# Optimization experiments

Measured on AMD Instinct MI355X. Metric: run time of the kernel, lower is better.

Reference implementation:

```python
import jax, jax.numpy as jnp
import numpy as np

B, T, D, H, FF, E = 4, 1024, 1024, 16, 4096, 8
HD = D // H
EPS = 1e-5


def layernorm(x, g, b):
    mu = jnp.mean(x, axis=-1, keepdims=True)
    var = jnp.mean(jnp.square(x - mu), axis=-1, keepdims=True)
    return (x - mu) * jax.lax.rsqrt(var + EPS) * g + b


def setup_inputs() -> dict:
    key = jax.random.key(0)
    ks = jax.random.split(key, 24)
    s = 0.02
    inp = {
        "src": jax.random.normal(ks[0], (B, T, D), jnp.float32),
        "frac": jax.random.uniform(ks[1], (B, T), jnp.float32),
        "Wq": jax.random.normal(ks[2], (D, D), jnp.float32) * s,
        "bq": jnp.zeros((D,), jnp.float32),
        "Wk": jax.random.normal(ks[3], (D, D), jnp.float32) * s,
        "bk": jnp.zeros((D,), jnp.float32),
        "Wv": jax.random.normal(ks[4], (D, D), jnp.float32) * s,
        "bv": jnp.zeros((D,), jnp.float32),
        "Wo": jax.random.normal(ks[5], (D, D), jnp.float32) * s,
        "bo": jnp.zeros((D,), jnp.float32),
        "alpha_pos": jax.random.normal(ks[6], (H,), jnp.float32) * s,
        "alpha_neg": jax.random.normal(ks[7], (H,), jnp.float32) * s,
        "gate_W": jax.random.normal(ks[8], (D, E), jnp.float32) * s,
        "gate_b": jnp.zeros((E,), jnp.float32),
        "W1": jax.random.normal(ks[9], (E, D, FF), jnp.float32) * s,
        "b1": jnp.zeros((E, FF), jnp.float32),
        "W2": jax.random.normal(ks[10], (E, FF, D), jnp.float32) * s,
        "b2": jnp.zeros((E, D), jnp.float32),
        "ln1_g": jnp.ones((D,), jnp.float32),
        "ln1_b": jnp.zeros((D,), jnp.float32),
        "ln2_g": jnp.ones((D,), jnp.float32),
        "ln2_b": jnp.zeros((D,), jnp.float32),
    }
    return inp


def reference(src, frac, Wq, bq, Wk, bk, Wv, bv, Wo, bo, alpha_pos, alpha_neg,
              gate_W, gate_b, W1, b1, W2, b2, ln1_g, ln1_b, ln2_g, ln2_b):
    # ---- attention with per-head stoichiometric bias ----
    q = (src @ Wq + bq).reshape(B, T, H, HD).transpose(0, 2, 1, 3)  # [B,H,T,hd]
    k = (src @ Wk + bk).reshape(B, T, H, HD).transpose(0, 2, 1, 3)
    v = (src @ Wv + bv).reshape(B, T, H, HD).transpose(0, 2, 1, 3)
    scale = HD ** -0.5
    scores = jnp.einsum('bhqd,bhkd->bhqk', q, k) * scale  # [B,H,T,T]
    Dm = frac[:, None, :] - frac[:, :, None]  # frac_j - frac_i, [B,T,T]
    bias = (alpha_pos[None, :, None, None] * jax.nn.relu(Dm)[:, None]
            - alpha_neg[None, :, None, None] * jax.nn.relu(-Dm)[:, None])
    probs = jax.nn.softmax(scores + bias, axis=-1)
    attn = jnp.einsum('bhqk,bhkd->bhqd', probs, v)
    attn = attn.transpose(0, 2, 1, 3).reshape(B, T, D) @ Wo + bo

    x = layernorm(src + attn, ln1_g, ln1_b)

    # ---- top-2 MoE FFN ----
    logits = x @ gate_W + gate_b  # [B,T,E]
    gscores = jax.nn.softmax(logits, axis=-1)
    top2_scores, top2_idx = jax.lax.top_k(gscores, 2)  # [B,T,2]
    # dense per-expert combine weight: score if expert in top-2 else 0
    weights = jnp.sum(jax.nn.one_hot(top2_idx, E, dtype=x.dtype)
                      * top2_scores[..., None], axis=-2)  # [B,T,E]
    ff = jnp.zeros_like(x)
    for e in range(E):  # small fixed expert count
        h = jax.nn.relu(x @ W1[e] + b1[e])
        ff = ff + weights[..., e:e + 1] * (h @ W2[e] + b2[e])

    return layernorm(x + ff, ln2_g, ln2_b)
```

## Files before the change

### kernel.cpp

```cpp
#include <hip/hip_runtime.h>
#include <stdint.h>

typedef unsigned short u16;
typedef unsigned int   u32;

using bf16x8 = __attribute__((ext_vector_type(8))) short;
using f32x4  = __attribute__((ext_vector_type(4))) float;

#define N_T   1024
#define N_D   1024
#define N_E   8
#define N_BT  4096
#define LNEPS 1e-5f

__device__ __forceinline__ u32 rne2(float a, float b) {
  u32 ua = __float_as_uint(a); ua = (ua + 0x7fffu + ((ua >> 16) & 1u)) >> 16;
  u32 ub = __float_as_uint(b); ub = (ub + 0x7fffu + ((ub >> 16) & 1u)) >> 16;
  return ua | (ub << 16);
}
__device__ __forceinline__ u16 rne1(float a) {
  u32 ua = __float_as_uint(a);
  return (u16)((ua + 0x7fffu + ((ua >> 16) & 1u)) >> 16);
}
__device__ __forceinline__ float bfhi_f(float a) {
  u32 ua = __float_as_uint(a);
  ua = (ua + 0x7fffu + ((ua >> 16) & 1u)) & 0xffff0000u;
  return __uint_as_float(ua);
}
__device__ __forceinline__ int fch(int row) { return (row & 3) ^ ((row >> 2) & 3); }
__device__ __forceinline__ int swz(int row, int chunk) {
  return row * 32 + (((chunk ^ fch(row)) & 3) << 3);
}
__device__ __forceinline__ float wred(float v) {
  #pragma unroll
  for (int o2 = 32; o2 > 0; o2 >>= 1) v += __shfl_xor(v, o2, 64);
  return v;
}
__device__ __forceinline__ f32x4 mfma16(bf16x8 a, bf16x8 b, f32x4 c) {
  return __builtin_amdgcn_mfma_f32_16x16x32_bf16(a, b, c, 0, 0, 0);
}
typedef __attribute__((address_space(1))) const u32 gas_u32;
typedef __attribute__((address_space(3))) u32 las_u32;
__device__ __forceinline__ void gl16(const void* g, void* l) {
  __builtin_amdgcn_global_load_lds((gas_u32*)g, (las_u32*)l, 16, 0, 0);
}

template<int SPLIT>
__global__ __launch_bounds__(256)
void transpose_bf16(const float* __restrict__ in, u16* __restrict__ outh,
                    u16* __restrict__ outl, int R, int C, float scale)
{
  __shared__ u16 th[64][68];
  __shared__ u16 tl[SPLIT ? 64 : 1][SPLIT ? 68 : 1];
  const long long zb = (long long)blockIdx.z * R * C;
  const float* srcp = in + zb;
  const int r0 = blockIdx.y * 64, c0 = blockIdx.x * 64;
  const int t = threadIdx.x;
  {
    const int rr = t >> 4, cc = (t & 15) << 2;
    #pragma unroll
    for (int i = 0; i < 4; i++) {
      const int r = rr + i * 16;
      float4 v = *(const float4*)(srcp + (long long)(r0 + r) * C + c0 + cc);
      v.x *= scale; v.y *= scale; v.z *= scale; v.w *= scale;
      if constexpr (SPLIT) {
        float hx = bfhi_f(v.x), hy = bfhi_f(v.y), hz = bfhi_f(v.z), hw = bfhi_f(v.w);
        *(uint2*)&th[r][cc] = make_uint2(rne2(hx, hy), rne2(hz, hw));
        *(uint2*)&tl[r][cc] = make_uint2(rne2(v.x - hx, v.y - hy), rne2(v.z - hz, v.w - hw));
      } else {
        *(uint2*)&th[r][cc] = make_uint2(rne2(v.x, v.y), rne2(v.z, v.w));
      }
    }
  }
  __syncthreads();
  {
    const int c = t >> 2, rs = (t & 3) << 4;
    const long long ob = zb + (long long)(c0 + c) * R + r0 + rs;
    u32 w[8];
    #pragma unroll
    for (int i = 0; i < 8; i++)
      w[i] = (u32)th[rs + 2*i][c] | ((u32)th[rs + 2*i + 1][c] << 16);
    *(uint4*)(outh + ob)     = make_uint4(w[0], w[1], w[2], w[3]);
    *(uint4*)(outh + ob + 8) = make_uint4(w[4], w[5], w[6], w[7]);
    if constexpr (SPLIT) {
      #pragma unroll
      for (int i = 0; i < 8; i++)
        w[i] = (u32)tl[rs + 2*i][c] | ((u32)tl[rs + 2*i + 1][c] << 16);
      *(uint4*)(outl + ob)     = make_uint4(w[0], w[1], w[2], w[3]);
      *(uint4*)(outl + ob + 8) = make_uint4(w[4], w[5], w[6], w[7]);
    }
  }
}

__global__ __launch_bounds__(256)
void bias_cat(const float* __restrict__ bq, const float* __restrict__ bk,
              const float* __restrict__ bv, float* __restrict__ bcat)
{
  const int i = blockIdx.x * 256 + threadIdx.x;
  if (i < 1024)       bcat[i] = bq[i] * 0.125f;
  else if (i < 2048)  bcat[i] = bk[i - 1024];
  else if (i < 3072)  bcat[i] = bv[i - 2048];
}

__global__ __launch_bounds__(256)
void vtrans_bf16(const u16* __restrict__ Vh, const u16* __restrict__ Vl, int ldv,
                 u16* __restrict__ Vth, u16* __restrict__ Vtl)
{
  __shared__ u16 th[64][72];
  __shared__ u16 tl[64][72];
  const int bh = blockIdx.y, b = bh >> 4, h = bh & 15;
  const int kt = blockIdx.x, tid = threadIdx.x;
  {
    const int sr = tid >> 2, scb = (tid & 3) << 4;
    const long long off = (long long)(b * N_T + kt * 64 + sr) * ldv + h * 64 + scb;
    const uint4* vh = (const uint4*)(Vh + off);
    const uint4* vl = (const uint4*)(Vl + off);
    *(uint4*)&th[sr][scb]     = vh[0];
    *(uint4*)&th[sr][scb + 8] = vh[1];
    *(uint4*)&tl[sr][scb]     = vl[0];
    *(uint4*)&tl[sr][scb + 8] = vl[1];
  }
  __syncthreads();
  {
    const int od = tid >> 2, os0 = (tid & 3) << 4;
    u16 wh[16], wl[16];
    #pragma unroll
    for (int i = 0; i < 16; i++) { wh[i] = th[os0 + i][od]; wl[i] = tl[os0 + i][od]; }
    u16* oph = Vth + (long long)(bh * 64 + od) * N_T + kt * 64 + os0;
    u16* opl = Vtl + (long long)(bh * 64 + od) * N_T + kt * 64 + os0;
    *(uint4*)oph = make_uint4((u32)wh[0] | ((u32)wh[1] << 16), (u32)wh[2] | ((u32)wh[3] << 16),
                              (u32)wh[4] | ((u32)wh[5] << 16), (u32)wh[6] | ((u32)wh[7] << 16));
    *(uint4*)(oph + 8) = make_uint4((u32)wh[8] | ((u32)wh[9] << 16), (u32)wh[10] | ((u32)wh[11] << 16),
                                    (u32)wh[12] | ((u32)wh[13] << 16), (u32)wh[14] | ((u32)wh[15] << 16));
    *(uint4*)opl = make_uint4((u32)wl[0] | ((u32)wl[1] << 16), (u32)wl[2] | ((u32)wl[3] << 16),
                              (u32)wl[4] | ((u32)wl[5] << 16), (u32)wl[6] | ((u32)wl[7] << 16));
    *(uint4*)(opl + 8) = make_uint4((u32)wl[8] | ((u32)wl[9] << 16), (u32)wl[10] | ((u32)wl[11] << 16),
                                    (u32)wl[12] | ((u32)wl[13] << 16), (u32)wl[14] | ((u32)wl[15] << 16));
  }
}

template<int ASPLIT, int GATHER, int DORELU, int DOSCALE, int OBF, int GROUPED, int CG>
__global__ __launch_bounds__(256, 2)
void gemm128(const void* __restrict__ Ap, int lda,
             const u16* __restrict__ Bhp, const u16* __restrict__ Blp,
             long long bstride,
             void* __restrict__ Cp, int ldc,
             const float* __restrict__ biasp, int bias_stride,
             const float* __restrict__ slot_wp,
             const int* __restrict__ tokidx,
             const int2* __restrict__ tilesp, const int* __restrict__ ntilesp,
             int Ksz, void* __restrict__ Cp2, float cscale)
{
  const int gx = gridDim.x, nwg = gx * gridDim.y;
  const int orig = blockIdx.y * gx + blockIdx.x;
  const int flat = (orig & 7) * (nwg >> 3) + (orig >> 3);
  const int cgsz = gx * CG;
  const int colg = flat / cgsz, rem = flat % cgsz;
  const int bxx = rem / CG;
  const int byy = colg * CG + rem % CG;

  int e = 0, row0;
  if constexpr (GROUPED) {
    if (bxx >= *ntilesp) return;
    const int2 dsc = tilesp[bxx];
    e = dsc.x; row0 = dsc.y;
  } else {
    row0 = bxx * 128;
  }
  const int col0 = byy * 128;

  __shared__ __align__(16) u16 AhS[ASPLIT ? 1 : 2][128 * 32];
  __shared__ __align__(16) u16 BhS[ASPLIT ? 1 : 2][128 * 32];
  __shared__ __align__(16) u16 AlS[ASPLIT ? 128 * 32 : 8];
  __shared__ __align__(16) u16 BlS[ASPLIT ? 128 * 32 : 8];

  const int tid = threadIdx.x, wid = tid >> 6, lane = tid & 63;
  const int wm = (wid >> 1) << 6, wn = (wid & 1) << 6;
  const int l15 = lane & 15, l4 = lane >> 4;

  const int srow0 = wid * 32 + (lane >> 2);
  const int srow1 = srow0 + 16;
  const int sg0 = ((lane & 3) ^ fch(srow0)) << 3;
  const int sg1 = ((lane & 3) ^ fch(srow1)) << 3;
  const int lo0 = wid * 1024, lo1 = wid * 1024 + 512;

  const u16* Bg0 = Bhp + (long long)e * bstride + (long long)(col0 + srow0) * Ksz + sg0;
  const u16* Bg1 = Bhp + (long long)e * bstride + (long long)(col0 + srow1) * Ksz + sg1;
  const u16* Blg0 = nullptr; const u16* Blg1 = nullptr;
  if constexpr (ASPLIT) {
    Blg0 = Blp + (long long)e * bstride + (long long)(col0 + srow0) * Ksz + sg0;
    Blg1 = Blp + (long long)e * bstride + (long long)(col0 + srow1) * Ksz + sg1;
  }

  const u16* Ag0 = nullptr; const u16* Ag1 = nullptr;
  if constexpr (!ASPLIT) {
    long long ar0, ar1;
    if constexpr (GATHER) { ar0 = tokidx[row0 + srow0]; ar1 = tokidx[row0 + srow1]; }
    else                  { ar0 = row0 + srow0;          ar1 = row0 + srow1; }
    Ag0 = (const u16*)Ap + ar0 * (long long)lda + sg0;
    Ag1 = (const u16*)Ap + ar1 * (long long)lda + sg1;
  }

  f32x4 acc[4][4] = {};
  const int nk = Ksz >> 5;

  if constexpr (!ASPLIT) {
    gl16(Ag0, &AhS[0][lo0]); gl16(Ag1, &AhS[0][lo1]);
    gl16(Bg0, &BhS[0][lo0]); gl16(Bg1, &BhS[0][lo1]);
    asm volatile("s_waitcnt vmcnt(0)" ::: "memory");
    __syncthreads();
    int cur = 0;
    for (int kt = 0; kt < nk; kt++) {
      if (kt + 1 < nk) {
        const int ko = (kt + 1) << 5;
        gl16(Ag0 + ko, &AhS[cur ^ 1][lo0]);
        gl16(Ag1 + ko, &AhS[cur ^ 1][lo1]);
        gl16(Bg0 + ko, &BhS[cur ^ 1][lo0]);
        gl16(Bg1 + ko, &BhS[cur ^ 1][lo1]);
      }
      bf16x8 ah[4], bh[4];
      #pragma unroll
      for (int i = 0; i < 4; i++) {
        ah[i] = *(const bf16x8*)&AhS[cur][swz(wm + i * 16 + l15, l4)];
        bh[i] = *(const bf16x8*)&BhS[cur][swz(wn + i * 16 + l15, l4)];
      }
      #pragma unroll
      for (int i = 0; i < 4; i++)
        #pragma unroll
        for (int j = 0; j < 4; j++)
          acc[i][j] = mfma16(ah[i], bh[j], acc[i][j]);
      asm volatile("s_waitcnt vmcnt(0)" ::: "memory");
      __syncthreads();
      cur ^= 1;
    }
  } else {
    const int prr = tid >> 1, pc2 = (tid & 1) << 1;
    const float* Arow = (const float*)Ap + (long long)(row0 + prr) * lda;
    uint4 sah0, sah1, sal0, sal1;
    auto gloadA = [&](int k0) {
      const float4* ap = (const float4*)(Arow + k0 + pc2 * 8);
      float4 f0 = ap[0], f1 = ap[1], f2 = ap[2], f3 = ap[3];
      float h0 = bfhi_f(f0.x), h1 = bfhi_f(f0.y), h2 = bfhi_f(f0.z), h3 = bfhi_f(f0.w);
      float h4 = bfhi_f(f1.x), h5 = bfhi_f(f1.y), h6 = bfhi_f(f1.z), h7 = bfhi_f(f1.w);
      sah0 = make_uint4(rne2(h0, h1), rne2(h2, h3), rne2(h4, h5), rne2(h6, h7));
      sal0 = make_uint4(rne2(f0.x - h0, f0.y - h1), rne2(f0.z - h2, f0.w - h3),
                        rne2(f1.x - h4, f1.y - h5), rne2(f1.z - h6, f1.w - h7));
      h0 = bfhi_f(f2.x); h1 = bfhi_f(f2.y); h2 = bfhi_f(f2.z); h3 = bfhi_f(f2.w);
      h4 = bfhi_f(f3.x); h5 = bfhi_f(f3.y); h6 = bfhi_f(f3.z); h7 = bfhi_f(f3.w);
      sah1 = make_uint4(rne2(h0, h1), rne2(h2, h3), rne2(h4, h5), rne2(h6, h7));
      sal1 = make_uint4(rne2(f2.x - h0, f2.y - h1), rne2(f2.z - h2, f2.w - h3),
                        rne2(f3.x - h4, f3.y - h5), rne2(f3.z - h6, f3.w - h7));
    };
    gloadA(0);
    for (int kt = 0; kt < nk; kt++) {
      __syncthreads();
      const int ko = kt << 5;
      *(uint4*)&AhS[0][swz(prr, pc2)]     = sah0;
      *(uint4*)&AhS[0][swz(prr, pc2 + 1)] = sah1;
      *(uint4*)&AlS[swz(prr, pc2)]        = sal0;
      *(uint4*)&AlS[swz(prr, pc2 + 1)]    = sal1;
      gl16(Bg0 + ko, &BhS[0][lo0]);
      gl16(Bg1 + ko, &BhS[0][lo1]);
      gl16(Blg0 + ko, &BlS[lo0]);
      gl16(Blg1 + ko, &BlS[lo1]);
      asm volatile("s_waitcnt vmcnt(0)" ::: "memory");
      __syncthreads();
      if (kt + 1 < nk) gloadA((kt + 1) << 5);

      bf16x8 ah[4], bh[4], al[4], bl[4];
      #pragma unroll
      for (int i = 0; i < 4; i++) {
        const int ar = wm + i * 16 + l15;
        const int br = wn + i * 16 + l15;
        ah[i] = *(const bf16x8*)&AhS[0][swz(ar, l4)];
        bh[i] = *(const bf16x8*)&BhS[0][swz(br, l4)];
        al[i] = *(const bf16x8*)&AlS[swz(ar, l4)];
        bl[i] = *(const bf16x8*)&BlS[swz(br, l4)];
      }
      #pragma unroll
      for (int i = 0; i < 4; i++) {
        #pragma unroll
        for (int j = 0; j < 4; j++) {
          acc[i][j] = mfma16(ah[i], bh[j], acc[i][j]);
          acc[i][j] = mfma16(ah[i], bl[j], acc[i][j]);
          acc[i][j] = mfma16(al[i], bh[j], acc[i][j]);
        }
      }
    }
  }

  #pragma unroll
  for (int i = 0; i < 4; i++) {
    #pragma unroll
    for (int j = 0; j < 4; j++) {
      const int orow0 = row0 + wm + i * 16 + (l4 << 2);
      const int ocol  = col0 + wn + j * 16 + l15;
      const float bv = biasp[(long long)e * bias_stride + col0 + wn + j * 16 + l15];
      #pragma unroll
      for (int q = 0; q < 4; q++) {
        float v = acc[i][j][q] + bv;
        if constexpr (DORELU) v = fmaxf(v, 0.f);
        const long long orow = orow0 + q;
        if constexpr (DOSCALE) v *= slot_wp[orow];
        if constexpr (OBF == 2) {
          const float vs = v * cscale;
          const float hi = bfhi_f(vs);
          ((u16*)Cp )[orow * ldc + ocol] = (u16)(__float_as_uint(hi) >> 16);
          ((u16*)Cp2)[orow * ldc + ocol] = rne1(vs - hi);
        } else if constexpr (OBF == 1) {
          ((u16*)Cp)[orow * ldc + ocol] = rne1(v);
        } else {
          ((float*)Cp)[orow * ldc + ocol] = v;
        }
      }
    }
  }
}

__global__ __launch_bounds__(256, 2)
void attn_mfma(const u16* __restrict__ Qh, const u16* __restrict__ Ql,
               const u16* __restrict__ Kh, const u16* __restrict__ Kl, int ldq,
               const u16* __restrict__ Vth, const u16* __restrict__ Vtl,
               const float* __restrict__ frac,
               const float* __restrict__ apos, const float* __restrict__ aneg,
               float* __restrict__ ctx)
{
  __shared__ __align__(16) u16 KhS[64 * 64];
  __shared__ __align__(16) u16 KlS[64 * 64];
  __shared__ __align__(16) u16 VhS[64 * 64];
  __shared__ __align__(16) u16 VlS[64 * 64];
  __shared__ __align__(16) u16 PS[4][32][72];
  __shared__ __align__(16) float fjS[64];

  const int bh = blockIdx.x, b = bh >> 4, h = bh & 15;
  const int tid = threadIdx.x, wid = tid >> 6, lane = tid & 63;
  const int l15 = lane & 15, l4 = lane >> 4;
  const int q0 = blockIdx.y * 128 + wid * 32;

  bf16x8 qh[2][2], ql[2][2];
  #pragma unroll
  for (int ni = 0; ni < 2; ni++) {
    const long long qoff = (long long)(b * N_T + q0 + ni * 16 + l15) * ldq + h * 64 + l4 * 8;
    #pragma unroll
    for (int ks = 0; ks < 2; ks++) {
      qh[ni][ks] = *(const bf16x8*)(Qh + qoff + ks * 32);
      ql[ni][ks] = *(const bf16x8*)(Ql + qoff + ks * 32);
    }
  }
  float fq[2];
  #pragma unroll
  for (int ni = 0; ni < 2; ni++) fq[ni] = frac[b * N_T + q0 + ni * 16 + l15];
  const float ap = apos[h], an = aneg[h];

  f32x4 acc[4][2] = {};
  float mrun[2] = {-3.0e38f, -3.0e38f}, lrun[2] = {0.f, 0.f};

  const int sr = tid >> 2, scb = (tid & 3) << 4;
  const int ch0 = ((scb >> 3) ^ (sr & 7)) << 3;
  const int ch1 = (((scb >> 3) + 1) ^ (sr & 7)) << 3;

  for (int kt = 0; kt < 16; kt++) {
    __syncthreads();
    {
      const long long koff = (long long)(b * N_T + kt * 64 + sr) * ldq + h * 64 + scb;
      const uint4* khp = (const uint4*)(Kh + koff);
      const uint4* klp = (const uint4*)(Kl + koff);
      const long long voff = (long long)(bh * 64 + sr) * N_T + kt * 64 + scb;
      const uint4* vhp = (const uint4*)(Vth + voff);
      const uint4* vlp = (const uint4*)(Vtl + voff);
      *(uint4*)&KhS[sr * 64 + ch0] = khp[0];
      *(uint4*)&KhS[sr * 64 + ch1] = khp[1];
      *(uint4*)&KlS[sr * 64 + ch0] = klp[0];
      *(uint4*)&KlS[sr * 64 + ch1] = klp[1];
      *(uint4*)&VhS[sr * 64 + ch0] = vhp[0];
      *(uint4*)&VhS[sr * 64 + ch1] = vhp[1];
      *(uint4*)&VlS[sr * 64 + ch0] = vlp[0];
      *(uint4*)&VlS[sr * 64 + ch1] = vlp[1];
    }
    if (tid < 64) fjS[tid] = frac[b * N_T + kt * 64 + tid];
    __syncthreads();

    f32x4 s[4][2] = {};
    #pragma unroll
    for (int ks = 0; ks < 2; ks++) {
      bf16x8 kh[4], kl[4];
      #pragma unroll
      for (int mj = 0; mj < 4; mj++) {
        const int row = mj * 16 + l15;
        const int ch = (((ks << 2) + l4) ^ (row & 7)) << 3;
        kh[mj] = *(const bf16x8*)&KhS[row * 64 + ch];
        kl[mj] = *(const bf16x8*)&KlS[row * 64 + ch];
      }
      #pragma unroll
      for (int mj = 0; mj < 4; mj++) {
        #pragma unroll
        for (int ni = 0; ni < 2; ni++) {
          s[mj][ni] = mfma16(kh[mj], qh[ni][ks], s[mj][ni]);
          s[mj][ni] = mfma16(kh[mj], ql[ni][ks], s[mj][ni]);
          s[mj][ni] = mfma16(kl[mj], qh[ni][ks], s[mj][ni]);
        }
      }
    }

    #pragma unroll
    for (int mj = 0; mj < 4; mj++) {
      const int kvb = mj * 16 + l4 * 4;
      const float f0 = fjS[kvb], f1 = fjS[kvb + 1], f2 = fjS[kvb + 2], f3 = fjS[kvb + 3];
      #pragma unroll
      for (int ni = 0; ni < 2; ni++) {
        float d0 = f0 - fq[ni], d1 = f1 - fq[ni], d2 = f2 - fq[ni], d3 = f3 - fq[ni];
        s[mj][ni][0] += (d0 > 0.f ? ap : an) * d0;
        s[mj][ni][1] += (d1 > 0.f ? ap : an) * d1;
        s[mj][ni][2] += (d2 > 0.f ? ap : an) * d2;
        s[mj][ni][3] += (d3 > 0.f ? ap : an) * d3;
      }
    }

    #pragma unroll
    for (int ni = 0; ni < 2; ni++) {
      float tm = s[0][ni][0];
      #pragma unroll
      for (int mj = 0; mj < 4; mj++) {
        tm = fmaxf(tm, fmaxf(fmaxf(s[mj][ni][0], s[mj][ni][1]),
                             fmaxf(s[mj][ni][2], s[mj][ni][3])));
      }
      tm = fmaxf(tm, __shfl_xor(tm, 16, 64));
      tm = fmaxf(tm, __shfl_xor(tm, 32, 64));
      const float nm = fmaxf(mrun[ni], tm);
      const float cor = __expf(mrun[ni] - nm);
      mrun[ni] = nm;
      lrun[ni] *= cor;
      #pragma unroll
      for (int md = 0; md < 4; md++) {
        acc[md][ni][0] *= cor; acc[md][ni][1] *= cor;
        acc[md][ni][2] *= cor; acc[md][ni][3] *= cor;
      }
      float rsum = 0.f;
      #pragma unroll
      for (int mj = 0; mj < 4; mj++) {
        #pragma unroll
        for (int r = 0; r < 4; r++) {
          const float p = __expf(s[mj][ni][r] - nm);
          s[mj][ni][r] = p;
          rsum += p;
        }
      }
      rsum += __shfl_xor(rsum, 16, 64);
      rsum += __shfl_xor(rsum, 32, 64);
      lrun[ni] += rsum;
    }

    #pragma unroll
    for (int ni = 0; ni < 2; ni++) {
      #pragma unroll
      for (int mj = 0; mj < 4; mj++) {
        float h0 = bfhi_f(s[mj][ni][0]), h1 = bfhi_f(s[mj][ni][1]);
        float h2 = bfhi_f(s[mj][ni][2]), h3 = bfhi_f(s[mj][ni][3]);
        u32* dst = (u32*)&PS[wid][ni * 16 + l15][mj * 16 + l4 * 4];
        dst[0] = rne2(h0, h1); dst[1] = rne2(h2, h3);
      }
    }
    bf16x8 pbh[2][2];
    #pragma unroll
    for (int ni = 0; ni < 2; ni++)
      #pragma unroll
      for (int ks = 0; ks < 2; ks++)
        pbh[ni][ks] = *(const bf16x8*)&PS[wid][ni * 16 + l15][ks * 32 + l4 * 8];

    #pragma unroll
    for (int ni = 0; ni < 2; ni++) {
      #pragma unroll
      for (int mj = 0; mj < 4; mj++) {
        float p0 = s[mj][ni][0], p1 = s[mj][ni][1], p2 = s[mj][ni][2], p3 = s[mj][ni][3];
        float h0 = bfhi_f(p0), h1 = bfhi_f(p1), h2 = bfhi_f(p2), h3 = bfhi_f(p3);
        u32* dst = (u32*)&PS[wid][ni * 16 + l15][mj * 16 + l4 * 4];
        dst[0] = rne2(p0 - h0, p1 - h1); dst[1] = rne2(p2 - h2, p3 - h3);
      }
    }
    bf16x8 pbl[2][2];
    #pragma unroll
    for (int ni = 0; ni < 2; ni++)
      #pragma unroll
      for (int ks = 0; ks < 2; ks++)
        pbl[ni][ks] = *(const bf16x8*)&PS[wid][ni * 16 + l15][ks * 32 + l4 * 8];

    #pragma unroll
    for (int md = 0; md < 4; md++) {
      #pragma unroll
      for (int ks = 0; ks < 2; ks++) {
        const int row = md * 16 + l15;
        const int ch = (((ks << 2) + l4) ^ (row & 7)) << 3;
        const bf16x8 vh = *(const bf16x8*)&VhS[row * 64 + ch];
        const bf16x8 vl = *(const bf16x8*)&VlS[row * 64 + ch];
        #pragma unroll
        for (int nq = 0; nq < 2; nq++) {
          acc[md][nq] = mfma16(vh, pbh[nq][ks], acc[md][nq]);
          acc[md][nq] = mfma16(vh, pbl[nq][ks], acc[md][nq]);
          acc[md][nq] = mfma16(vl, pbh[nq][ks], acc[md][nq]);
        }
      }
    }
  }

  const float inv[2] = {1.f / lrun[0], 1.f / lrun[1]};
  #pragma unroll
  for (int nq = 0; nq < 2; nq++) {
    #pragma unroll
    for (int md = 0; md < 4; md++) {
      float4 o;
      o.x = acc[md][nq][0] * inv[nq];
      o.y = acc[md][nq][1] * inv[nq];
      o.z = acc[md][nq][2] * inv[nq];
      o.w = acc[md][nq][3] * inv[nq];
      *(float4*)(ctx + (long long)(b * N_T + q0 + nq * 16 + l15) * N_D +
                 h * 64 + md * 16 + l4 * 4) = o;
    }
  }
}

__global__ __launch_bounds__(256, 4)
void ln1_gate(const float* __restrict__ src, const float* __restrict__ attnout,
              const float* __restrict__ g, const float* __restrict__ bb,
              const float* __restrict__ gateW, const float* __restrict__ gateb,
              float* __restrict__ xout, u16* __restrict__ xbf,
              int2* __restrict__ tok_top, float2* __restrict__ tok_w)
{
  const int wid = threadIdx.x >> 6, lane = threadIdx.x & 63;
  const int t = blockIdx.x * 4 + wid;
  const float4* s4 = (const float4*)(src + (long long)t * N_D);
  const float4* a4 = (const float4*)(attnout + (long long)t * N_D);
  float4 v[4];
  float sum = 0.f;
  #pragma unroll
  for (int c = 0; c < 4; c++) {
    const int idx = c * 64 + lane;
    float4 a = s4[idx], b2 = a4[idx];
    v[c] = make_float4(a.x + b2.x, a.y + b2.y, a.z + b2.z, a.w + b2.w);
    sum += v[c].x + v[c].y + v[c].z + v[c].w;
  }
  sum = wred(sum);
  const float mu = sum * (1.f / 1024.f);
  float s2 = 0.f;
  #pragma unroll
  for (int c = 0; c < 4; c++) {
    float dx = v[c].x - mu, dy = v[c].y - mu, dz = v[c].z - mu, dw = v[c].w - mu;
    s2 += dx * dx + dy * dy + dz * dz + dw * dw;
  }
  s2 = wred(s2);
  const float rs = rsqrtf(s2 * (1.f / 1024.f) + LNEPS);
  float acc[8];
  #pragma unroll
  for (int e2 = 0; e2 < 8; e2++) acc[e2] = 0.f;
  #pragma unroll
  for (int c = 0; c < 4; c++) {
    const int idx = c * 64 + lane;
    float4 gv = ((const float4*)g)[idx], bv = ((const float4*)bb)[idx];
    float xa[4];
    xa[0] = (v[c].x - mu) * rs * gv.x + bv.x;
    xa[1] = (v[c].y - mu) * rs * gv.y + bv.y;
    xa[2] = (v[c].z - mu) * rs * gv.z + bv.z;
    xa[3] = (v[c].w - mu) * rs * gv.w + bv.w;
    ((float4*)(xout + (long long)t * N_D))[idx] = make_float4(xa[0], xa[1], xa[2], xa[3]);
    *(uint2*)&xbf[(long long)t * N_D + idx * 4] =
        make_uint2(rne2(xa[0], xa[1]), rne2(xa[2], xa[3]));
    #pragma unroll
    for (int ii = 0; ii < 4; ii++) {
      const float xs = xa[ii];
      const float4* gw = (const float4*)(gateW + ((long long)(idx * 4 + ii)) * N_E);
      float4 w0 = gw[0], w1 = gw[1];
      acc[0] += xs * w0.x; acc[1] += xs * w0.y; acc[2] += xs * w0.z; acc[3] += xs * w0.w;
      acc[4] += xs * w1.x; acc[5] += xs * w1.y; acc[6] += xs * w1.z; acc[7] += xs * w1.w;
    }
  }
  #pragma unroll
  for (int e2 = 0; e2 < 8; e2++) acc[e2] = wred(acc[e2]);
  if (lane == 0) {
    float lg[8];
    #pragma unroll
    for (int e2 = 0; e2 < 8; e2++) lg[e2] = acc[e2] + gateb[e2];
    float mx = lg[0];
    #pragma unroll
    for (int e2 = 1; e2 < 8; e2++) mx = fmaxf(mx, lg[e2]);
    float Z = 0.f;
    #pragma unroll
    for (int e2 = 0; e2 < 8; e2++) Z += __expf(lg[e2] - mx);
    int e0 = 0; float v0 = lg[0];
    #pragma unroll
    for (int e2 = 1; e2 < 8; e2++) if (lg[e2] > v0) { v0 = lg[e2]; e0 = e2; }
    int e1 = -1; float v1 = -3.4e38f;
    #pragma unroll
    for (int e2 = 0; e2 < 8; e2++) if (e2 != e0 && lg[e2] > v1) { v1 = lg[e2]; e1 = e2; }
    tok_top[t] = make_int2(e0, e1);
    tok_w[t] = make_float2(__expf(v0 - mx) / Z, __expf(v1 - mx) / Z);
  }
}

__global__ __launch_bounds__(256)
void route_build(const int2* __restrict__ tok_top, int* __restrict__ offsets,
                 int* __restrict__ cursors, int* __restrict__ ntiles,
                 int2* __restrict__ tiles, int* __restrict__ token_idx,
                 float* __restrict__ slot_w)
{
  __shared__ int cnt[N_E];
  __shared__ int soff[N_E + 1];
  __shared__ int scnt[N_E];
  const int tid = threadIdx.x;
  if (tid < N_E) cnt[tid] = 0;
  __syncthreads();
  int lc0 = 0, lc1 = 0, lc2 = 0, lc3 = 0, lc4 = 0, lc5 = 0, lc6 = 0, lc7 = 0;
  for (int t = tid; t < N_BT; t += 256) {
    const int2 ee = tok_top[t];
    lc0 += (ee.x == 0) + (ee.y == 0); lc1 += (ee.x == 1) + (ee.y == 1);
    lc2 += (ee.x == 2) + (ee.y == 2); lc3 += (ee.x == 3) + (ee.y == 3);
    lc4 += (ee.x == 4) + (ee.y == 4); lc5 += (ee.x == 5) + (ee.y == 5);
    lc6 += (ee.x == 6) + (ee.y == 6); lc7 += (ee.x == 7) + (ee.y == 7);
  }
  if (lc0) atomicAdd(&cnt[0], lc0); if (lc1) atomicAdd(&cnt[1], lc1);
  if (lc2) atomicAdd(&cnt[2], lc2); if (lc3) atomicAdd(&cnt[3], lc3);
  if (lc4) atomicAdd(&cnt[4], lc4); if (lc5) atomicAdd(&cnt[5], lc5);
  if (lc6) atomicAdd(&cnt[6], lc6); if (lc7) atomicAdd(&cnt[7], lc7);
  __syncthreads();
  if (tid == 0) {
    int off = 0, nt = 0;
    for (int ex = 0; ex < N_E; ex++) {
      soff[ex] = off; offsets[ex] = off; cursors[ex] = 0;
      const int c = cnt[ex];
      scnt[ex] = c;
      const int pt = (c + 127) >> 7;
      for (int i = 0; i < pt; i++) { tiles[nt] = make_int2(ex, off + i * 128); nt++; }
      off += pt << 7;
    }
    soff[N_E] = off; offsets[N_E] = off;
    *ntiles = nt;
  }
  __syncthreads();
  for (int ex = 0; ex < N_E; ex++)
    for (int s = soff[ex] + scnt[ex] + tid; s < soff[ex + 1]; s += 256) {
      token_idx[s] = 0; slot_w[s] = 0.f;
    }
}

__global__ __launch_bounds__(256)
void route_scatter(const int2* __restrict__ tok_top, const float2* __restrict__ tok_w,
                   const int* __restrict__ offsets, int* __restrict__ cursors,
                   int* __restrict__ token_idx, float* __restrict__ slot_w,
                   int* __restrict__ slotA, int* __restrict__ slotB)
{
  const int t = blockIdx.x * 256 + threadIdx.x;
  if (t >= N_BT) return;
  const int2 ee = tok_top[t];
  const float2 ww = tok_w[t];
  int p = atomicAdd(&cursors[ee.x], 1);
  int s = offsets[ee.x] + p;
  token_idx[s] = t; slot_w[s] = ww.x; slotA[t] = s;
  p = atomicAdd(&cursors[ee.y], 1);
  s = offsets[ee.y] + p;
  token_idx[s] = t; slot_w[s] = ww.y; slotB[t] = s;
}

__global__ __launch_bounds__(256, 4)
void final_ln2(const float* __restrict__ x, const float* __restrict__ out2,
               const int* __restrict__ slotA, const int* __restrict__ slotB,
               const float* __restrict__ g, const float* __restrict__ bb,
               float* __restrict__ out)
{
  const int wid = threadIdx.x >> 6, lane = threadIdx.x & 63;
  const int t = blockIdx.x * 4 + wid;
  const int sA = slotA[t], sB = slotB[t];
  const float4* xr = (const float4*)(x + (long long)t * N_D);
  const float4* pa = (const float4*)(out2 + (long long)sA * N_D);
  const float4* pb = (const float4*)(out2 + (long long)sB * N_D);
  float4 v[4];
  float sum = 0.f;
  #pragma unroll
  for (int c = 0; c < 4; c++) {
    const int idx = c * 64 + lane;
    float4 a = xr[idx], b2 = pa[idx], c2 = pb[idx];
    v[c] = make_float4(a.x + b2.x + c2.x, a.y + b2.y + c2.y,
                       a.z + b2.z + c2.z, a.w + b2.w + c2.w);
    sum += v[c].x + v[c].y + v[c].z + v[c].w;
  }
  sum = wred(sum);
  const float mu = sum * (1.f / 1024.f);
  float s2 = 0.f;
  #pragma unroll
  for (int c = 0; c < 4; c++) {
    float dx = v[c].x - mu, dy = v[c].y - mu, dz = v[c].z - mu, dw = v[c].w - mu;
    s2 += dx * dx + dy * dy + dz * dz + dw * dw;
  }
  s2 = wred(s2);
  const float rs = rsqrtf(s2 * (1.f / 1024.f) + LNEPS);
  #pragma unroll
  for (int c = 0; c < 4; c++) {
    const int idx = c * 64 + lane;
    float4 gv = ((const float4*)g)[idx], bv = ((const float4*)bb)[idx];
    float4 o;
    o.x = (v[c].x - mu) * rs * gv.x + bv.x;
    o.y = (v[c].y - mu) * rs * gv.y + bv.y;
    o.z = (v[c].z - mu) * rs * gv.z + bv.z;
    o.w = (v[c].w - mu) * rs * gv.w + bv.w;
    ((float4*)(out + (long long)t * N_D))[idx] = o;
  }
}

extern "C" void kernel_launch(void* const* d_in, const int* in_sizes, int n_in,
                              void* d_out, int out_size, void* d_ws, size_t ws_size,
                              hipStream_t stream)
{
  const float* src   = (const float*)d_in[0];
  const float* frac  = (const float*)d_in[1];
  const float* Wq    = (const float*)d_in[2];
  const float* bq    = (const float*)d_in[3];
  const float* Wk    = (const float*)d_in[4];
  const float* bk    = (const float*)d_in[5];
  const float* Wv    = (const float*)d_in[6];
  const float* bv    = (const float*)d_in[7];
  const float* Wo    = (const float*)d_in[8];
  const float* bo    = (const float*)d_in[9];
  const float* apos  = (const float*)d_in[10];
  const float* aneg  = (const float*)d_in[11];
  const float* gateW = (const float*)d_in[12];
  const float* gateb = (const float*)d_in[13];
  const float* W1    = (const float*)d_in[14];
  const float* b1    = (const float*)d_in[15];
  const float* W2    = (const float*)d_in[16];
  const float* b2    = (const float*)d_in[17];
  const float* ln1g  = (const float*)d_in[18];
  const float* ln1b  = (const float*)d_in[19];
  const float* ln2g  = (const float*)d_in[20];
  const float* ln2b  = (const float*)d_in[21];
  float* out = (float*)d_out;

  char* ws = (char*)d_ws;
  const size_t MB = 1ull << 20;
  u16* Bcath = (u16*)(ws + 0 * MB);
  u16* Bcatl = (u16*)(ws + 6 * MB);
  u16* WoTh  = (u16*)(ws + 12 * MB);
  u16* WoTl  = (u16*)(ws + 14 * MB);
  u16*   W1T  = (u16*)(ws + 16 * MB);
  float* out2 = (float*)(ws + 16 * MB);
  u16*   W2T  = (u16*)(ws + 80 * MB);
  u16*   QKVh = (u16*)(ws + 144 * MB);
  u16*   QKVl = (u16*)(ws + 168 * MB);
  u16*   Vth  = (u16*)(ws + 192 * MB);
  u16*   Vtl  = (u16*)(ws + 200 * MB);
  float* ctxb = (float*)(ws + 208 * MB);
  float* attnb= (float*)(ws + 144 * MB);
  u16*   hb   = (u16*)(ws + 144 * MB);
  float* xb   = (float*)(ws + 224 * MB);
  u16*   xbf  = (u16*)(ws + 4 * MB);
  float* bcat = (float*)(ws + 240 * MB);
  char* misc = ws + 0;
  int*    cursors   = (int*)(misc + 64);
  int*    offsets   = (int*)(misc + 128);
  int*    ntiles    = (int*)(misc + 256);
  int2*   tiles     = (int2*)(misc + 512);
  int2*   tok_top   = (int2*)(misc + 2048);
  float2* tok_w     = (float2*)(misc + 2048 + 32768);
  int*    token_idx = (int*)(misc + 2048 + 65536);
  float*  slot_w    = (float*)(misc + 2048 + 65536 + 36864);
  int*    slotA     = (int*)(misc + 2048 + 65536 + 73728);
  int*    slotB     = (int*)(misc + 2048 + 65536 + 73728 + 16384);

  dim3 b256(256);
  transpose_bf16<1><<<dim3(16, 16, 1), b256, 0, stream>>>(Wq, Bcath, Bcatl,
                                                          1024, 1024, 0.125f);
  transpose_bf16<1><<<dim3(16, 16, 1), b256, 0, stream>>>(Wk, Bcath + 1024 * 1024,
                                                          Bcatl + 1024 * 1024, 1024, 1024, 1.0f);
  transpose_bf16<1><<<dim3(16, 16, 1), b256, 0, stream>>>(Wv, Bcath + 2048 * 1024,
                                                          Bcatl + 2048 * 1024, 1024, 1024, 1.0f);
  transpose_bf16<1><<<dim3(16, 16, 1), b256, 0, stream>>>(Wo, WoTh, WoTl, 1024, 1024, 1.0f);
  transpose_bf16<0><<<dim3(64, 16, 8), b256, 0, stream>>>(W1, W1T, nullptr, 1024, 4096, 1.0f);
  transpose_bf16<0><<<dim3(16, 64, 8), b256, 0, stream>>>(W2, W2T, nullptr, 4096, 1024, 1.0f);
  bias_cat<<<dim3(12), b256, 0, stream>>>(bq, bk, bv, bcat);

  gemm128<1, 0, 0, 0, 2, 0, 3><<<dim3(32, 24), b256, 0, stream>>>(
      src, 1024, Bcath, Bcatl, 0, QKVh, 3072, bcat, 0, nullptr, nullptr, nullptr, nullptr,
      1024, QKVl, 1.0f);

  vtrans_bf16<<<dim3(16, 64), b256, 0, stream>>>(QKVh + 2048, QKVl + 2048, 3072, Vth, Vtl);

  attn_mfma<<<dim3(64, 8), b256, 0, stream>>>(QKVh, QKVl, QKVh + 1024, QKVl + 1024, 3072,
                                              Vth, Vtl, frac, apos, aneg, ctxb);

  gemm128<1, 0, 0, 0, 0, 0, 1><<<dim3(32, 8), b256, 0, stream>>>(
      ctxb, 1024, WoTh, WoTl, 0, attnb, 1024, bo, 0, nullptr, nullptr, nullptr, nullptr,
      1024, nullptr, 1.0f);

  ln1_gate<<<dim3(1024), b256, 0, stream>>>(src, attnb, ln1g, ln1b, gateW, gateb,
                                            xb, xbf, tok_top, tok_w);
  route_build<<<dim3(1), b256, 0, stream>>>(tok_top, offsets, cursors, ntiles,
                                            tiles, token_idx, slot_w);
  route_scatter<<<dim3(16), b256, 0, stream>>>(tok_top, tok_w, offsets, cursors,
                                               token_idx, slot_w, slotA, slotB);

  gemm128<0, 1, 1, 0, 1, 1, 4><<<dim3(72, 32), b256, 0, stream>>>(
      xbf, 1024, W1T, nullptr, 4096ll * 1024, hb, 4096, b1, 4096,
      nullptr, token_idx, tiles, ntiles, 1024, nullptr, 1.0f);
  gemm128<0, 0, 0, 1, 0, 1, 8><<<dim3(72, 8), b256, 0, stream>>>(
      hb, 4096, W2T, nullptr, 1024ll * 4096, out2, 1024, b2, 1024,
      slot_w, nullptr, tiles, ntiles, 4096, nullptr, 1.0f);

  final_ln2<<<dim3(1024), b256, 0, stream>>>(xb, out2, slotA, slotB, ln2g, ln2b, out);
}
```

Measured before the change: 600.4 us.

## Triple-buffer bf16 GEMM mainloop and merge four weight transposes into one launch

The non-split GEMM path moves from double to triple buffering in LDS. Loads are issued two k-tiles ahead, and each step waits with vmcnt(4) instead of draining all outstanding loads, so global latency overlaps more MFMA work. The four separate Wq/Wk/Wv/Wo split-transpose launches are also fused into one grid with z selecting the matrix, which saves launch overhead. The extra LDS buffer raises shared memory use per block and may lower occupancy.

```diff
diff --git a/kernel.cpp b/kernel.cpp
--- a/kernel.cpp
+++ b/kernel.cpp
@@ -89,6 +89,51 @@
       *(uint4*)(outl + ob)     = make_uint4(w[0], w[1], w[2], w[3]);
       *(uint4*)(outl + ob + 8) = make_uint4(w[4], w[5], w[6], w[7]);
     }
+  }
+}
+
+__global__ __launch_bounds__(256)
+void trans4(const float* __restrict__ Wq, const float* __restrict__ Wk,
+            const float* __restrict__ Wv, const float* __restrict__ Wo,
+            u16* __restrict__ Bcath, u16* __restrict__ Bcatl,
+            u16* __restrict__ WoTh, u16* __restrict__ WoTl)
+{
+  __shared__ u16 th[64][68];
+  __shared__ u16 tl[64][68];
+  const int z = blockIdx.z;
+  const float* in = (z == 0) ? Wq : (z == 1) ? Wk : (z == 2) ? Wv : Wo;
+  u16* outh = (z == 3) ? WoTh : (Bcath + (long long)z * 1024 * 1024);
+  u16* outl = (z == 3) ? WoTl : (Bcatl + (long long)z * 1024 * 1024);
+  const float scale = (z == 0) ? 0.125f : 1.0f;
+  const int r0 = blockIdx.y * 64, c0 = blockIdx.x * 64;
+  const int t = threadIdx.x;
+  {
+    const int rr = t >> 4, cc = (t & 15) << 2;
+    #pragma unroll
+    for (int i = 0; i < 4; i++) {
+      const int r = rr + i * 16;
+      float4 v = *(const float4*)(in + (long long)(r0 + r) * 1024 + c0 + cc);
+      v.x *= scale; v.y *= scale; v.z *= scale; v.w *= scale;
+      float hx = bfhi_f(v.x), hy = bfhi_f(v.y), hz = bfhi_f(v.z), hw = bfhi_f(v.w);
+      *(uint2*)&th[r][cc] = make_uint2(rne2(hx, hy), rne2(hz, hw));
+      *(uint2*)&tl[r][cc] = make_uint2(rne2(v.x - hx, v.y - hy), rne2(v.z - hz, v.w - hw));
+    }
+  }
+  __syncthreads();
+  {
+    const int c = t >> 2, rs = (t & 3) << 4;
+    const long long ob = (long long)(c0 + c) * 1024 + r0 + rs;
+    u32 w[8];
+    #pragma unroll
+    for (int i = 0; i < 8; i++)
+      w[i] = (u32)th[rs + 2*i][c] | ((u32)th[rs + 2*i + 1][c] << 16);
+    *(uint4*)(outh + ob)     = make_uint4(w[0], w[1], w[2], w[3]);
+    *(uint4*)(outh + ob + 8) = make_uint4(w[4], w[5], w[6], w[7]);
+    #pragma unroll
+    for (int i = 0; i < 8; i++)
+      w[i] = (u32)tl[rs + 2*i][c] | ((u32)tl[rs + 2*i + 1][c] << 16);
+    *(uint4*)(outl + ob)     = make_uint4(w[0], w[1], w[2], w[3]);
+    *(uint4*)(outl + ob + 8) = make_uint4(w[4], w[5], w[6], w[7]);
   }
 }
 
@@ -169,8 +214,8 @@
   }
   const int col0 = byy * 128;
 
-  __shared__ __align__(16) u16 AhS[ASPLIT ? 1 : 2][128 * 32];
-  __shared__ __align__(16) u16 BhS[ASPLIT ? 1 : 2][128 * 32];
+  __shared__ __align__(16) u16 AhS[ASPLIT ? 1 : 3][128 * 32];
+  __shared__ __align__(16) u16 BhS[ASPLIT ? 1 : 3][128 * 32];
   __shared__ __align__(16) u16 AlS[ASPLIT ? 128 * 32 : 8];
   __shared__ __align__(16) u16 BlS[ASPLIT ? 128 * 32 : 8];
 
@@ -207,31 +252,33 @@
   if constexpr (!ASPLIT) {
     gl16(Ag0, &AhS[0][lo0]); gl16(Ag1, &AhS[0][lo1]);
     gl16(Bg0, &BhS[0][lo0]); gl16(Bg1, &BhS[0][lo1]);
-    asm volatile("s_waitcnt vmcnt(0)" ::: "memory");
-    __syncthreads();
-    int cur = 0;
+    gl16(Ag0 + 32, &AhS[1][lo0]); gl16(Ag1 + 32, &AhS[1][lo1]);
+    gl16(Bg0 + 32, &BhS[1][lo0]); gl16(Bg1 + 32, &BhS[1][lo1]);
     for (int kt = 0; kt < nk; kt++) {
-      if (kt + 1 < nk) {
-        const int ko = (kt + 1) << 5;
-        gl16(Ag0 + ko, &AhS[cur ^ 1][lo0]);
-        gl16(Ag1 + ko, &AhS[cur ^ 1][lo1]);
-        gl16(Bg0 + ko, &BhS[cur ^ 1][lo0]);
-        gl16(Bg1 + ko, &BhS[cur ^ 1][lo1]);
-      }
+      if (kt + 1 < nk) asm volatile("s_waitcnt vmcnt(4)" ::: "memory");
+      else             asm volatile("s_waitcnt vmcnt(0)" ::: "memory");
+      __syncthreads();
+      const int bi = kt % 3;
       bf16x8 ah[4], bh[4];
       #pragma unroll
       for (int i = 0; i < 4; i++) {
-        ah[i] = *(const bf16x8*)&AhS[cur][swz(wm + i * 16 + l15, l4)];
-        bh[i] = *(const bf16x8*)&BhS[cur][swz(wn + i * 16 + l15, l4)];
+        ah[i] = *(const bf16x8*)&AhS[bi][swz(wm + i * 16 + l15, l4)];
+        bh[i] = *(const bf16x8*)&BhS[bi][swz(wn + i * 16 + l15, l4)];
       }
       #pragma unroll
       for (int i = 0; i < 4; i++)
         #pragma unroll
         for (int j = 0; j < 4; j++)
           acc[i][j] = mfma16(ah[i], bh[j], acc[i][j]);
-      asm volatile("s_waitcnt vmcnt(0)" ::: "memory");
       __syncthreads();
-      cur ^= 1;
+      if (kt + 2 < nk) {
+        const int ko = (kt + 2) << 5;
+        const int bn = (kt + 2) % 3;
+        gl16(Ag0 + ko, &AhS[bn][lo0]);
+        gl16(Ag1 + ko, &AhS[bn][lo1]);
+        gl16(Bg0 + ko, &BhS[bn][lo0]);
+        gl16(Bg1 + ko, &BhS[bn][lo1]);
+      }
     }
   } else {
     const int prr = tid >> 1, pc2 = (tid & 1) << 1;
@@ -763,13 +810,7 @@
   int*    slotB     = (int*)(misc + 2048 + 65536 + 73728 + 16384);
 
   dim3 b256(256);
-  transpose_bf16<1><<<dim3(16, 16, 1), b256, 0, stream>>>(Wq, Bcath, Bcatl,
-                                                          1024, 1024, 0.125f);
-  transpose_bf16<1><<<dim3(16, 16, 1), b256, 0, stream>>>(Wk, Bcath + 1024 * 1024,
-                                                          Bcatl + 1024 * 1024, 1024, 1024, 1.0f);
-  transpose_bf16<1><<<dim3(16, 16, 1), b256, 0, stream>>>(Wv, Bcath + 2048 * 1024,
-                                                          Bcatl + 2048 * 1024, 1024, 1024, 1.0f);
-  transpose_bf16<1><<<dim3(16, 16, 1), b256, 0, stream>>>(Wo, WoTh, WoTl, 1024, 1024, 1.0f);
+  trans4<<<dim3(16, 16, 4), b256, 0, stream>>>(Wq, Wk, Wv, Wo, Bcath, Bcatl, WoTh, WoTl);
   transpose_bf16<0><<<dim3(64, 16, 8), b256, 0, stream>>>(W1, W1T, nullptr, 1024, 4096, 1.0f);
   transpose_bf16<0><<<dim3(16, 64, 8), b256, 0, stream>>>(W2, W2T, nullptr, 4096, 1024, 1.0f);
   bias_cat<<<dim3(12), b256, 0, stream>>>(bq, bk, bv, bcat);
```

Result: no change. 611.7 us (+1.9%).
